# Kernel tuning notes

Measured on AMD Instinct MI355X. Metric: run time of the kernel, lower is better.

The kernel has to match this reference:

```python
import jax, jax.numpy as jnp
import numpy as np

N = 200000
E = 600000
C = 256


def setup_inputs() -> dict:
    key = jax.random.key(0)
    k1, k2, k3, k4, k5 = jax.random.split(key, 5)
    x = jax.random.normal(k1, (N, C), dtype=jnp.float32)
    sources = jax.random.randint(k2, (E,), 0, N, dtype=jnp.int64)
    targets = jax.random.randint(k3, (E,), 0, N, dtype=jnp.int64)
    norm = jax.random.uniform(k4, (N, 1), dtype=jnp.float32)
    # xavier_normal for [C, C]: std = sqrt(2 / (fan_in + fan_out))
    std = float(np.sqrt(2.0 / (C + C)))
    weight = jax.random.normal(k5, (C, C), dtype=jnp.float32) * std
    return {"x": x, "sources": sources, "targets": targets, "norm": norm, "weight": weight}


def reference(x, sources, targets, norm, weight):
    # out-of-place index_add: x + scatter_add(x[sources] -> targets)
    agg = x.at[targets].add(x[sources])  # [N, C]
    h = norm * agg                        # [N, C], norm broadcasts over channels
    return h @ weight                     # [N, C]
```

## Files before the change

### kernel.cpp

```cpp
#include <hip/hip_runtime.h>
#include <hip/hip_bf16.h>

#define NN 200000
#define NE 600000
#define CH 256
#define NBLK_SCAN 196

typedef short bf16x8 __attribute__((ext_vector_type(8)));
typedef float f32x4 __attribute__((ext_vector_type(4)));
typedef unsigned short ushort8v __attribute__((ext_vector_type(8)));

__device__ __forceinline__ unsigned short f2bf(float f) {
    unsigned int u = __builtin_bit_cast(unsigned int, f);
    u = (u + 0x7FFFu + ((u >> 16) & 1u)) >> 16;
    return (unsigned short)u;
}
__device__ __forceinline__ float bf2f(unsigned short u) {
    unsigned int v = ((unsigned int)u) << 16;
    return __builtin_bit_cast(float, v);
}

__global__ __launch_bounds__(256) void k_prep(const float* __restrict__ W,
                                              unsigned short* __restrict__ Wt,
                                              const int* __restrict__ te,
                                              int* __restrict__ deg) {
    const int t = blockIdx.x * 256 + threadIdx.x;
    const int S = gridDim.x * 256;
    for (int e = t; e < NE; e += S) atomicAdd(&deg[te[e]], 1);
    for (int i = t; i < CH * CH; i += S) {
        int j = i >> 8, k = i & 255;
        Wt[j * CH + k] = f2bf(W[k * CH + j]);
    }
}

__global__ __launch_bounds__(256) void k_scanA(const int* __restrict__ deg,
                                               int* __restrict__ off,
                                               int* __restrict__ bsum) {
    __shared__ int ts[256];
    int tid = threadIdx.x;
    int base = blockIdx.x * 1024 + tid * 4;
    int v[4];
#pragma unroll
    for (int j = 0; j < 4; ++j) {
        int idx = base + j;
        v[j] = (idx < NN) ? deg[idx] : 0;
    }
    int tsum = v[0] + v[1] + v[2] + v[3];
    ts[tid] = tsum;
    __syncthreads();
    int x = tsum;
    for (int ofs = 1; ofs < 256; ofs <<= 1) {
        int y = (tid >= ofs) ? ts[tid - ofs] : 0;
        __syncthreads();
        x += y;
        ts[tid] = x;
        __syncthreads();
    }
    int run = x - tsum;
#pragma unroll
    for (int j = 0; j < 4; ++j) {
        int idx = base + j;
        if (idx < NN) off[idx] = run;
        run += v[j];
    }
    if (tid == 255) bsum[blockIdx.x] = x;
}

__global__ __launch_bounds__(256) void k_scanB(int* __restrict__ bsum) {
    __shared__ int ts[256];
    int tid = threadIdx.x;
    int v = (tid < NBLK_SCAN) ? bsum[tid] : 0;
    ts[tid] = v;
    __syncthreads();
    int x = v;
    for (int ofs = 1; ofs < 256; ofs <<= 1) {
        int y = (tid >= ofs) ? ts[tid - ofs] : 0;
        __syncthreads();
        x += y;
        ts[tid] = x;
        __syncthreads();
    }
    if (tid < NBLK_SCAN) bsum[tid] = x - v;
}

__global__ __launch_bounds__(256) void k_scanC(int* __restrict__ off,
                                               const int* __restrict__ bsum,
                                               int* __restrict__ cur) {
    int tid = threadIdx.x;
    int base = blockIdx.x * 1024 + tid * 4;
    int bo = bsum[blockIdx.x];
#pragma unroll
    for (int j = 0; j < 4; ++j) {
        int idx = base + j;
        if (idx < NN) {
            int o = off[idx] + bo;
            off[idx] = o;
            cur[idx] = o;
        }
    }
}

__global__ void k_fill(const int* __restrict__ se, const int* __restrict__ te,
                       int* __restrict__ cur, int* __restrict__ elist) {
    int e = blockIdx.x * 256 + threadIdx.x;
    if (e < NE) {
        int t = te[e];
        int pos = atomicAdd(&cur[t], 1);
        elist[pos] = se[e];
    }
}

__global__ __launch_bounds__(256, 2) void k_zw(const float* __restrict__ x,
                                               const unsigned short* __restrict__ Wt,
                                               unsigned short* __restrict__ zbf) {
    __shared__ unsigned short lds_a[64 * CH];
    const int tid = threadIdx.x;
    const int wid = tid >> 6;
    const int lane = tid & 63;
    const int rb = blockIdx.x * 64;
    const int r16 = lane & 15;
    const int q = lane >> 4;

    const float* gx = x + (size_t)rb * CH;
#pragma unroll
    for (int i = 0; i < 8; ++i) {
        const int idx = i * 2048 + tid * 8;
        const int row = idx >> 8;
        const int col = idx & 255;
        float4 f0 = *reinterpret_cast<const float4*>(gx + idx);
        float4 f1 = *reinterpret_cast<const float4*>(gx + idx + 4);
        ushort8v w;
        w[0] = f2bf(f0.x); w[1] = f2bf(f0.y); w[2] = f2bf(f0.z); w[3] = f2bf(f0.w);
        w[4] = f2bf(f1.x); w[5] = f2bf(f1.y); w[6] = f2bf(f1.z); w[7] = f2bf(f1.w);
        const int gs = (col >> 3) ^ (row & 7);
        *reinterpret_cast<ushort8v*>(&lds_a[row * CH + gs * 8]) = w;
    }
    __syncthreads();

    f32x4 acc[4][4];
#pragma unroll
    for (int m = 0; m < 4; ++m)
#pragma unroll
        for (int nt = 0; nt < 4; ++nt) acc[m][nt] = (f32x4){0.f, 0.f, 0.f, 0.f};

    const unsigned short* wb = Wt + (size_t)(wid * 64 + r16) * CH + q * 8;

#pragma unroll
    for (int kk = 0; kk < 8; ++kk) {
        bf16x8 b[4];
#pragma unroll
        for (int nt = 0; nt < 4; ++nt)
            b[nt] = *reinterpret_cast<const bf16x8*>(wb + (size_t)nt * 16 * CH + kk * 32);
        bf16x8 a[4];
#pragma unroll
        for (int m = 0; m < 4; ++m) {
            const int lr = m * 16 + r16;
            const int idx = lr * CH + ((((kk * 4) + q) ^ (lr & 7)) << 3);
            a[m] = *reinterpret_cast<const bf16x8*>(&lds_a[idx]);
        }
#pragma unroll
        for (int m = 0; m < 4; ++m)
#pragma unroll
            for (int nt = 0; nt < 4; ++nt)
                acc[m][nt] = __builtin_amdgcn_mfma_f32_16x16x32_bf16(a[m], b[nt], acc[m][nt], 0, 0, 0);
    }

#pragma unroll
    for (int m = 0; m < 4; ++m) {
        const int crow = rb + m * 16 + q * 4;
#pragma unroll
        for (int nt = 0; nt < 4; ++nt) {
            unsigned short* po = zbf + (size_t)crow * CH + wid * 64 + nt * 16 + r16;
#pragma unroll
            for (int r = 0; r < 4; ++r) po[(size_t)r * CH] = f2bf(acc[m][nt][r]);
        }
    }
}

__global__ __launch_bounds__(256) void k_gout(const unsigned short* __restrict__ zbf,
                                              const int* __restrict__ off,
                                              const int* __restrict__ deg,
                                              const int* __restrict__ elist,
                                              const float* __restrict__ norm,
                                              float* __restrict__ out) {
    int wid = threadIdx.x >> 6;
    int lane = threadIdx.x & 63;
    int row = blockIdx.x * 4 + wid;
    if (row >= NN) return;
    int start = off[row];
    int d = deg[row];
    const int uo = lane * 4;
    ushort4 bv = *reinterpret_cast<const ushort4*>(zbf + (size_t)row * CH + uo);
    float ax = bf2f(bv.x), ay = bf2f(bv.y), az = bf2f(bv.z), aw = bf2f(bv.w);
    int e = 0;
    while (e < d) {
        int i0 = (e + 0 < d) ? elist[start + e + 0] : -1;
        int i1 = (e + 1 < d) ? elist[start + e + 1] : -1;
        int i2 = (e + 2 < d) ? elist[start + e + 2] : -1;
        int i3 = (e + 3 < d) ? elist[start + e + 3] : -1;
        int i4 = (e + 4 < d) ? elist[start + e + 4] : -1;
        int i5 = (e + 5 < d) ? elist[start + e + 5] : -1;
        int i6 = (e + 6 < d) ? elist[start + e + 6] : -1;
        int i7 = (e + 7 < d) ? elist[start + e + 7] : -1;
#define GACC(ii) if (ii >= 0) { \
            ushort4 v = *reinterpret_cast<const ushort4*>(zbf + (size_t)ii * CH + uo); \
            ax += bf2f(v.x); ay += bf2f(v.y); az += bf2f(v.z); aw += bf2f(v.w); }
        GACC(i0) GACC(i1) GACC(i2) GACC(i3) GACC(i4) GACC(i5) GACC(i6) GACC(i7)
#undef GACC
        e += 8;
    }
    const float nv = norm[row];
    float4 o;
    o.x = ax * nv; o.y = ay * nv; o.z = az * nv; o.w = aw * nv;
    *reinterpret_cast<float4*>(out + (size_t)row * CH + uo) = o;
}

__global__ __launch_bounds__(256, 4) void k_fgg(const float* __restrict__ x,
                                                const int* __restrict__ off,
                                                const int* __restrict__ deg,
                                                const int* __restrict__ elist,
                                                const float* __restrict__ norm,
                                                const unsigned short* __restrict__ Wt,
                                                float* __restrict__ out) {
    __shared__ unsigned short lds_a[64 * CH];
    const int tid = threadIdx.x;
    const int wid = tid >> 6;
    const int lane = tid & 63;
    const int rb = blockIdx.x * 64;
    const int rowbase = rb + wid * 16;
    const int r16 = lane & 15;
    const int q = lane >> 4;
    const int fo4 = lane * 4;

    const int offv = off[rowbase + r16];
    const int degv = deg[rowbase + r16];
    const float nv = norm[rb + lane];

    float4 acc[16];
#pragma unroll
    for (int r = 0; r < 16; ++r)
        acc[r] = *reinterpret_cast<const float4*>(x + (size_t)(rowbase + r) * CH + fo4);

#pragma unroll
    for (int r = 0; r < 16; ++r) {
        const int start = __shfl(offv, r);
        const int d = __shfl(degv, r);
        int e = 0;
        while (e < d) {
            int i0 = (e + 0 < d) ? elist[start + e + 0] : -1;
            int i1 = (e + 1 < d) ? elist[start + e + 1] : -1;
            int i2 = (e + 2 < d) ? elist[start + e + 2] : -1;
            int i3 = (e + 3 < d) ? elist[start + e + 3] : -1;
#define GACC(ii) if (ii >= 0) { \
            float4 v = *reinterpret_cast<const float4*>(x + (size_t)ii * CH + fo4); \
            acc[r].x += v.x; acc[r].y += v.y; acc[r].z += v.z; acc[r].w += v.w; }
            GACC(i0) GACC(i1) GACC(i2) GACC(i3)
#undef GACC
            e += 4;
        }
    }

    unsigned short* lb = lds_a + wid * 16 * CH;
#pragma unroll
    for (int r = 0; r < 16; ++r) {
        ushort4 w;
        w.x = f2bf(acc[r].x); w.y = f2bf(acc[r].y);
        w.z = f2bf(acc[r].z); w.w = f2bf(acc[r].w);
        const int gs = (lane >> 1) ^ (r & 7);
        *reinterpret_cast<ushort4*>(lb + r * CH + gs * 8 + (lane & 1) * 4) = w;
    }
    __syncthreads();

    f32x4 facc[4][4];
#pragma unroll
    for (int m = 0; m < 4; ++m)
#pragma unroll
        for (int nt = 0; nt < 4; ++nt) facc[m][nt] = (f32x4){0.f, 0.f, 0.f, 0.f};

    const unsigned short* wb = Wt + (size_t)(wid * 64 + r16) * CH + q * 8;

#pragma unroll
    for (int kk = 0; kk < 8; ++kk) {
        bf16x8 b[4];
#pragma unroll
        for (int nt = 0; nt < 4; ++nt)
            b[nt] = *reinterpret_cast<const bf16x8*>(wb + (size_t)nt * 16 * CH + kk * 32);
        bf16x8 a[4];
#pragma unroll
        for (int m = 0; m < 4; ++m) {
            const int lr = m * 16 + r16;
            const int idx = lr * CH + ((((kk * 4) + q) ^ (lr & 7)) << 3);
            a[m] = *reinterpret_cast<const bf16x8*>(&lds_a[idx]);
        }
#pragma unroll
        for (int m = 0; m < 4; ++m)
#pragma unroll
            for (int nt = 0; nt < 4; ++nt)
                facc[m][nt] = __builtin_amdgcn_mfma_f32_16x16x32_bf16(a[m], b[nt], facc[m][nt], 0, 0, 0);
    }

#pragma unroll
    for (int m = 0; m < 4; ++m) {
        const int crow = rb + m * 16 + q * 4;
#pragma unroll
        for (int nt = 0; nt < 4; ++nt) {
            float* po = out + (size_t)crow * CH + wid * 64 + nt * 16 + r16;
#pragma unroll
            for (int r = 0; r < 4; ++r) {
                const float nj = __shfl(nv, m * 16 + q * 4 + r);
                po[(size_t)r * CH] = facc[m][nt][r] * nj;
            }
        }
    }
}

extern "C" void kernel_launch(void* const* d_in, const int* in_sizes, int n_in,
                              void* d_out, int out_size, void* d_ws, size_t ws_size,
                              hipStream_t stream) {
    const float* x = (const float*)d_in[0];
    const int* se = (const int*)d_in[1];
    const int* te = (const int*)d_in[2];
    const float* norm = (const float*)d_in[3];
    const float* W = (const float*)d_in[4];
    float* out = (float*)d_out;

    char* ws = (char*)d_ws;
    unsigned short* Wt = (unsigned short*)ws;
    int* deg   = (int*)(ws + 131072);
    int* off   = (int*)(ws + 931072);
    int* cur   = (int*)(ws + 1731072);
    int* elist = (int*)(ws + 2531072);
    int* bsum  = (int*)(ws + 4931072);
    const size_t ZBF_OFF = 4932096;
    const size_t NEED = ZBF_OFF + (size_t)NN * CH * 2;
    const bool big = (ws_size >= NEED);
    unsigned short* zbf = (unsigned short*)(ws + ZBF_OFF);

    hipMemsetAsync(deg, 0, NN * sizeof(int), stream);
    k_prep<<<512, 256, 0, stream>>>(W, Wt, te, deg);
    k_scanA<<<NBLK_SCAN, 256, 0, stream>>>(deg, off, bsum);
    k_scanB<<<1, 256, 0, stream>>>(bsum);
    k_scanC<<<NBLK_SCAN, 256, 0, stream>>>(off, bsum, cur);
    k_fill<<<(NE + 255) / 256, 256, 0, stream>>>(se, te, cur, elist);
    if (big) {
        k_zw<<<NN / 64, 256, 0, stream>>>(x, Wt, zbf);
        k_gout<<<NN / 4, 256, 0, stream>>>(zbf, off, deg, elist, norm, out);
    } else {
        k_fgg<<<NN / 64, 256, 0, stream>>>(x, off, deg, elist, norm, Wt, out);
    }
}
```

Measured before the change: 279.1 us.

## Fold block-sum scan into scanC and double-buffer operand loads in k_zw

Removes the single-block k_scanB launch: each k_scanC block now redundantly scans all block sums in LDS and picks its own offset. k_zw issues all of its global x loads up front before converting them, and double-buffers the A (LDS) and B (global) MFMA operands across k-steps. Its occupancy hint is also raised from 2 to 3 waves. The aim is to cut one kernel launch and to hide load latency in the GEMM, at the cost of more registers that may not fit the higher occupancy target.

```diff
diff --git a/kernel.cpp b/kernel.cpp
--- a/kernel.cpp
+++ b/kernel.cpp
@@ -66,7 +66,9 @@
     if (tid == 255) bsum[blockIdx.x] = x;
 }
 
-__global__ __launch_bounds__(256) void k_scanB(int* __restrict__ bsum) {
+__global__ __launch_bounds__(256) void k_scanC(int* __restrict__ off,
+                                               const int* __restrict__ bsum,
+                                               int* __restrict__ cur) {
     __shared__ int ts[256];
     int tid = threadIdx.x;
     int v = (tid < NBLK_SCAN) ? bsum[tid] : 0;
@@ -80,15 +82,8 @@
         ts[tid] = x;
         __syncthreads();
     }
-    if (tid < NBLK_SCAN) bsum[tid] = x - v;
-}
-
-__global__ __launch_bounds__(256) void k_scanC(int* __restrict__ off,
-                                               const int* __restrict__ bsum,
-                                               int* __restrict__ cur) {
-    int tid = threadIdx.x;
+    const int bo = (blockIdx.x == 0) ? 0 : ts[blockIdx.x - 1];
     int base = blockIdx.x * 1024 + tid * 4;
-    int bo = bsum[blockIdx.x];
 #pragma unroll
     for (int j = 0; j < 4; ++j) {
         int idx = base + j;
@@ -110,7 +105,7 @@
     }
 }
 
-__global__ __launch_bounds__(256, 2) void k_zw(const float* __restrict__ x,
+__global__ __launch_bounds__(256, 3) void k_zw(const float* __restrict__ x,
                                                const unsigned short* __restrict__ Wt,
                                                unsigned short* __restrict__ zbf) {
     __shared__ unsigned short lds_a[64 * CH];
@@ -122,48 +117,62 @@
     const int q = lane >> 4;
 
     const float* gx = x + (size_t)rb * CH;
+    float4 st[16];
+#pragma unroll
+    for (int i = 0; i < 8; ++i) {
+        const int idx = i * 2048 + tid * 8;
+        st[2 * i]     = *reinterpret_cast<const float4*>(gx + idx);
+        st[2 * i + 1] = *reinterpret_cast<const float4*>(gx + idx + 4);
+    }
 #pragma unroll
     for (int i = 0; i < 8; ++i) {
         const int idx = i * 2048 + tid * 8;
         const int row = idx >> 8;
         const int col = idx & 255;
-        float4 f0 = *reinterpret_cast<const float4*>(gx + idx);
-        float4 f1 = *reinterpret_cast<const float4*>(gx + idx + 4);
         ushort8v w;
-        w[0] = f2bf(f0.x); w[1] = f2bf(f0.y); w[2] = f2bf(f0.z); w[3] = f2bf(f0.w);
-        w[4] = f2bf(f1.x); w[5] = f2bf(f1.y); w[6] = f2bf(f1.z); w[7] = f2bf(f1.w);
+        w[0] = f2bf(st[2 * i].x); w[1] = f2bf(st[2 * i].y);
+        w[2] = f2bf(st[2 * i].z); w[3] = f2bf(st[2 * i].w);
+        w[4] = f2bf(st[2 * i + 1].x); w[5] = f2bf(st[2 * i + 1].y);
+        w[6] = f2bf(st[2 * i + 1].z); w[7] = f2bf(st[2 * i + 1].w);
         const int gs = (col >> 3) ^ (row & 7);
         *reinterpret_cast<ushort8v*>(&lds_a[row * CH + gs * 8]) = w;
     }
     __syncthreads();
 
+    const unsigned short* wb = Wt + (size_t)(wid * 64 + r16) * CH + q * 8;
+#define LOADB(nt, kk) (*reinterpret_cast<const bf16x8*>(wb + (size_t)(nt) * 16 * CH + (kk) * 32))
+#define LOADA(m, kk) (*reinterpret_cast<const bf16x8*>(&lds_a[(m * 16 + r16) * CH + (((((kk) * 4) + q) ^ ((m * 16 + r16) & 7)) << 3)]))
+
+    bf16x8 ab[2][4], bb[2][4];
+#pragma unroll
+    for (int nt = 0; nt < 4; ++nt) bb[0][nt] = LOADB(nt, 0);
+#pragma unroll
+    for (int m = 0; m < 4; ++m) ab[0][m] = LOADA(m, 0);
+
     f32x4 acc[4][4];
 #pragma unroll
     for (int m = 0; m < 4; ++m)
 #pragma unroll
         for (int nt = 0; nt < 4; ++nt) acc[m][nt] = (f32x4){0.f, 0.f, 0.f, 0.f};
 
-    const unsigned short* wb = Wt + (size_t)(wid * 64 + r16) * CH + q * 8;
-
 #pragma unroll
     for (int kk = 0; kk < 8; ++kk) {
-        bf16x8 b[4];
-#pragma unroll
-        for (int nt = 0; nt < 4; ++nt)
-            b[nt] = *reinterpret_cast<const bf16x8*>(wb + (size_t)nt * 16 * CH + kk * 32);
-        bf16x8 a[4];
-#pragma unroll
-        for (int m = 0; m < 4; ++m) {
-            const int lr = m * 16 + r16;
-            const int idx = lr * CH + ((((kk * 4) + q) ^ (lr & 7)) << 3);
-            a[m] = *reinterpret_cast<const bf16x8*>(&lds_a[idx]);
+        const int cur = kk & 1;
+        const int nxt = cur ^ 1;
+        if (kk < 7) {
+#pragma unroll
+            for (int nt = 0; nt < 4; ++nt) bb[nxt][nt] = LOADB(nt, kk + 1);
+#pragma unroll
+            for (int m = 0; m < 4; ++m) ab[nxt][m] = LOADA(m, kk + 1);
         }
 #pragma unroll
         for (int m = 0; m < 4; ++m)
 #pragma unroll
             for (int nt = 0; nt < 4; ++nt)
-                acc[m][nt] = __builtin_amdgcn_mfma_f32_16x16x32_bf16(a[m], b[nt], acc[m][nt], 0, 0, 0);
-    }
+                acc[m][nt] = __builtin_amdgcn_mfma_f32_16x16x32_bf16(ab[cur][m], bb[cur][nt], acc[m][nt], 0, 0, 0);
+    }
+#undef LOADB
+#undef LOADA
 
 #pragma unroll
     for (int m = 0; m < 4; ++m) {
@@ -339,7 +348,6 @@
     hipMemsetAsync(deg, 0, NN * sizeof(int), stream);
     k_prep<<<512, 256, 0, stream>>>(W, Wt, te, deg);
     k_scanA<<<NBLK_SCAN, 256, 0, stream>>>(deg, off, bsum);
-    k_scanB<<<1, 256, 0, stream>>>(bsum);
     k_scanC<<<NBLK_SCAN, 256, 0, stream>>>(off, bsum, cur);
     k_fill<<<(NE + 255) / 256, 256, 0, stream>>>(se, te, cur, elist);
     if (big) {
```

After: 280.3 us. Within noise of the previous version (+0.4%).

## Fuse degree counting into GEMM, merge scan passes, widen GEMM tiles

Applied to the files above, without the earlier changes.

Folds the separate block-sum scan kernel into the final scan pass, with each block redoing the small 196-entry scan in LDS. Moves the edge-degree atomics into the z=xW GEMM kernel and splits the weight transpose into its own small kernel. Widens the GEMM block to 128 rows and 512 threads and stages the bf16 output through LDS for coalesced 16-byte stores. The goal is fewer launches and better store efficiency, at the cost of higher LDS use per block (64 KB), which may limit occupancy.

```diff
diff --git a/kernel.cpp b/kernel.cpp
--- a/kernel.cpp
+++ b/kernel.cpp
@@ -18,6 +18,11 @@
 __device__ __forceinline__ float bf2f(unsigned short u) {
     unsigned int v = ((unsigned int)u) << 16;
     return __builtin_bit_cast(float, v);
+}
+
+__global__ void k_wt(const float* __restrict__ W, unsigned short* __restrict__ Wt) {
+    int j = blockIdx.x, k = threadIdx.x;
+    Wt[j * CH + k] = f2bf(W[k * CH + j]);
 }
 
 __global__ __launch_bounds__(256) void k_prep(const float* __restrict__ W,
@@ -66,7 +71,9 @@
     if (tid == 255) bsum[blockIdx.x] = x;
 }
 
-__global__ __launch_bounds__(256) void k_scanB(int* __restrict__ bsum) {
+__global__ __launch_bounds__(256) void k_scanC(int* __restrict__ off,
+                                               const int* __restrict__ bsum,
+                                               int* __restrict__ cur) {
     __shared__ int ts[256];
     int tid = threadIdx.x;
     int v = (tid < NBLK_SCAN) ? bsum[tid] : 0;
@@ -80,15 +87,8 @@
         ts[tid] = x;
         __syncthreads();
     }
-    if (tid < NBLK_SCAN) bsum[tid] = x - v;
-}
-
-__global__ __launch_bounds__(256) void k_scanC(int* __restrict__ off,
-                                               const int* __restrict__ bsum,
-                                               int* __restrict__ cur) {
-    int tid = threadIdx.x;
+    const int bo = (blockIdx.x == 0) ? 0 : ts[blockIdx.x - 1];
     int base = blockIdx.x * 1024 + tid * 4;
-    int bo = bsum[blockIdx.x];
 #pragma unroll
     for (int j = 0; j < 4; ++j) {
         int idx = base + j;
@@ -110,25 +110,36 @@
     }
 }
 
-__global__ __launch_bounds__(256, 2) void k_zw(const float* __restrict__ x,
+__global__ __launch_bounds__(512, 4) void k_zw(const float* __restrict__ x,
                                                const unsigned short* __restrict__ Wt,
-                                               unsigned short* __restrict__ zbf) {
-    __shared__ unsigned short lds_a[64 * CH];
+                                               unsigned short* __restrict__ zbf,
+                                               const int* __restrict__ te,
+                                               int* __restrict__ deg) {
+    __shared__ unsigned short lds_a[128 * CH];
     const int tid = threadIdx.x;
     const int wid = tid >> 6;
     const int lane = tid & 63;
-    const int rb = blockIdx.x * 64;
+    const int wr = wid >> 2;
+    const int wc = wid & 3;
+    const int rb = blockIdx.x * 128;
     const int r16 = lane & 15;
     const int q = lane >> 4;
-
-    const float* gx = x + (size_t)rb * CH;
+    const int vr = min(128, NN - rb);
+
+    {
+        const long long e = (long long)blockIdx.x * 512 + tid;
+        if (e < NE) atomicAdd(&deg[te[e]], 1);
+    }
+
 #pragma unroll
     for (int i = 0; i < 8; ++i) {
-        const int idx = i * 2048 + tid * 8;
+        const int idx = i * 4096 + tid * 8;
         const int row = idx >> 8;
         const int col = idx & 255;
-        float4 f0 = *reinterpret_cast<const float4*>(gx + idx);
-        float4 f1 = *reinterpret_cast<const float4*>(gx + idx + 4);
+        const int srow = min(rb + row, NN - 1);
+        const float* src = x + (size_t)srow * CH + col;
+        float4 f0 = *reinterpret_cast<const float4*>(src);
+        float4 f1 = *reinterpret_cast<const float4*>(src + 4);
         ushort8v w;
         w[0] = f2bf(f0.x); w[1] = f2bf(f0.y); w[2] = f2bf(f0.z); w[3] = f2bf(f0.w);
         w[4] = f2bf(f1.x); w[5] = f2bf(f1.y); w[6] = f2bf(f1.z); w[7] = f2bf(f1.w);
@@ -143,7 +154,7 @@
 #pragma unroll
         for (int nt = 0; nt < 4; ++nt) acc[m][nt] = (f32x4){0.f, 0.f, 0.f, 0.f};
 
-    const unsigned short* wb = Wt + (size_t)(wid * 64 + r16) * CH + q * 8;
+    const unsigned short* wb = Wt + (size_t)(wc * 64 + r16) * CH + q * 8;
 
 #pragma unroll
     for (int kk = 0; kk < 8; ++kk) {
@@ -154,9 +165,9 @@
         bf16x8 a[4];
 #pragma unroll
         for (int m = 0; m < 4; ++m) {
-            const int lr = m * 16 + r16;
-            const int idx = lr * CH + ((((kk * 4) + q) ^ (lr & 7)) << 3);
-            a[m] = *reinterpret_cast<const bf16x8*>(&lds_a[idx]);
+            const int lr = wr * 64 + m * 16 + r16;
+            const int aidx = lr * CH + ((((kk * 4) + q) ^ (lr & 7)) << 3);
+            a[m] = *reinterpret_cast<const bf16x8*>(&lds_a[aidx]);
         }
 #pragma unroll
         for (int m = 0; m < 4; ++m)
@@ -165,15 +176,27 @@
                 acc[m][nt] = __builtin_amdgcn_mfma_f32_16x16x32_bf16(a[m], b[nt], acc[m][nt], 0, 0, 0);
     }
 
+    __syncthreads();
 #pragma unroll
     for (int m = 0; m < 4; ++m) {
-        const int crow = rb + m * 16 + q * 4;
 #pragma unroll
         for (int nt = 0; nt < 4; ++nt) {
-            unsigned short* po = zbf + (size_t)crow * CH + wid * 64 + nt * 16 + r16;
-#pragma unroll
-            for (int r = 0; r < 4; ++r) po[(size_t)r * CH] = f2bf(acc[m][nt][r]);
-        }
+            const int zr = wr * 64 + m * 16 + q * 4;
+            const int zc = wc * 64 + nt * 16 + r16;
+#pragma unroll
+            for (int r = 0; r < 4; ++r)
+                lds_a[(zr + r) * CH + zc] = f2bf(acc[m][nt][r]);
+        }
+    }
+    __syncthreads();
+    unsigned short* zdst = zbf + (size_t)rb * CH;
+#pragma unroll
+    for (int j = 0; j < 8; ++j) {
+        const int idx = j * 4096 + tid * 8;
+        const int row = idx >> 8;
+        if (row < vr)
+            *reinterpret_cast<ushort8v*>(zdst + idx) =
+                *reinterpret_cast<const ushort8v*>(&lds_a[idx]);
     }
 }
 
@@ -337,15 +360,18 @@
     unsigned short* zbf = (unsigned short*)(ws + ZBF_OFF);
 
     hipMemsetAsync(deg, 0, NN * sizeof(int), stream);
-    k_prep<<<512, 256, 0, stream>>>(W, Wt, te, deg);
-    k_scanA<<<NBLK_SCAN, 256, 0, stream>>>(deg, off, bsum);
-    k_scanB<<<1, 256, 0, stream>>>(bsum);
-    k_scanC<<<NBLK_SCAN, 256, 0, stream>>>(off, bsum, cur);
-    k_fill<<<(NE + 255) / 256, 256, 0, stream>>>(se, te, cur, elist);
     if (big) {
-        k_zw<<<NN / 64, 256, 0, stream>>>(x, Wt, zbf);
+        k_wt<<<CH, CH, 0, stream>>>(W, Wt);
+        k_zw<<<(NN + 127) / 128, 512, 0, stream>>>(x, Wt, zbf, te, deg);
+        k_scanA<<<NBLK_SCAN, 256, 0, stream>>>(deg, off, bsum);
+        k_scanC<<<NBLK_SCAN, 256, 0, stream>>>(off, bsum, cur);
+        k_fill<<<(NE + 255) / 256, 256, 0, stream>>>(se, te, cur, elist);
         k_gout<<<NN / 4, 256, 0, stream>>>(zbf, off, deg, elist, norm, out);
     } else {
+        k_prep<<<512, 256, 0, stream>>>(W, Wt, te, deg);
+        k_scanA<<<NBLK_SCAN, 256, 0, stream>>>(deg, off, bsum);
+        k_scanC<<<NBLK_SCAN, 256, 0, stream>>>(off, bsum, cur);
+        k_fill<<<(NE + 255) / 256, 256, 0, stream>>>(se, te, cur, elist);
         k_fgg<<<NN / 64, 256, 0, stream>>>(x, off, deg, elist, norm, Wt, out);
     }
 }
```

Result: faster. 263.2 us (-5.7%).

## Persistent double-buffered x@W GEMM with fused degree count and merged scan

Applied to the files above, without the earlier changes.

Turns k_zw into a persistent kernel of 512 blocks that loops over 32-row tiles. Each next tile of x is staged into LDS with async global_load_lds double buffering, the W fragments stay in registers for the whole kernel, and fp32 is converted to bf16 at LDS read time. Degree counting moves into the GEMM kernel so the atomics overlap with the GEMM. The separate scanB launch is removed by having each scanC block redo the small block-sum scan, and the W transpose becomes its own tiny kernel. This cuts launches and the exposed load latency, at the cost of heavy register use (32 bf16x8 B fragments) and twice the LDS footprint from keeping fp32 tiles.

```diff
diff --git a/kernel.cpp b/kernel.cpp
--- a/kernel.cpp
+++ b/kernel.cpp
@@ -5,6 +5,8 @@
 #define NE 600000
 #define CH 256
 #define NBLK_SCAN 196
+#define ZW_GRID 512
+#define ZW_TILES 6250
 
 typedef short bf16x8 __attribute__((ext_vector_type(8)));
 typedef float f32x4 __attribute__((ext_vector_type(4)));
@@ -18,6 +20,11 @@
 __device__ __forceinline__ float bf2f(unsigned short u) {
     unsigned int v = ((unsigned int)u) << 16;
     return __builtin_bit_cast(float, v);
+}
+
+__global__ void k_wt(const float* __restrict__ W, unsigned short* __restrict__ Wt) {
+    int j = blockIdx.x, k = threadIdx.x;
+    Wt[j * CH + k] = f2bf(W[k * CH + j]);
 }
 
 __global__ __launch_bounds__(256) void k_prep(const float* __restrict__ W,
@@ -66,7 +73,9 @@
     if (tid == 255) bsum[blockIdx.x] = x;
 }
 
-__global__ __launch_bounds__(256) void k_scanB(int* __restrict__ bsum) {
+__global__ __launch_bounds__(256) void k_scanC(int* __restrict__ off,
+                                               const int* __restrict__ bsum,
+                                               int* __restrict__ cur) {
     __shared__ int ts[256];
     int tid = threadIdx.x;
     int v = (tid < NBLK_SCAN) ? bsum[tid] : 0;
@@ -80,15 +89,8 @@
         ts[tid] = x;
         __syncthreads();
     }
-    if (tid < NBLK_SCAN) bsum[tid] = x - v;
-}
-
-__global__ __launch_bounds__(256) void k_scanC(int* __restrict__ off,
-                                               const int* __restrict__ bsum,
-                                               int* __restrict__ cur) {
-    int tid = threadIdx.x;
+    const int bo = (blockIdx.x == 0) ? 0 : ts[blockIdx.x - 1];
     int base = blockIdx.x * 1024 + tid * 4;
-    int bo = bsum[blockIdx.x];
 #pragma unroll
     for (int j = 0; j < 4; ++j) {
         int idx = base + j;
@@ -112,69 +114,97 @@
 
 __global__ __launch_bounds__(256, 2) void k_zw(const float* __restrict__ x,
                                                const unsigned short* __restrict__ Wt,
-                                               unsigned short* __restrict__ zbf) {
-    __shared__ unsigned short lds_a[64 * CH];
+                                               unsigned short* __restrict__ zbf,
+                                               const int* __restrict__ te,
+                                               int* __restrict__ deg) {
+    __shared__ float lds[2][32 * CH];
     const int tid = threadIdx.x;
     const int wid = tid >> 6;
     const int lane = tid & 63;
-    const int rb = blockIdx.x * 64;
     const int r16 = lane & 15;
     const int q = lane >> 4;
 
-    const float* gx = x + (size_t)rb * CH;
-#pragma unroll
-    for (int i = 0; i < 8; ++i) {
-        const int idx = i * 2048 + tid * 8;
-        const int row = idx >> 8;
-        const int col = idx & 255;
-        float4 f0 = *reinterpret_cast<const float4*>(gx + idx);
-        float4 f1 = *reinterpret_cast<const float4*>(gx + idx + 4);
-        ushort8v w;
-        w[0] = f2bf(f0.x); w[1] = f2bf(f0.y); w[2] = f2bf(f0.z); w[3] = f2bf(f0.w);
-        w[4] = f2bf(f1.x); w[5] = f2bf(f1.y); w[6] = f2bf(f1.z); w[7] = f2bf(f1.w);
-        const int gs = (col >> 3) ^ (row & 7);
-        *reinterpret_cast<ushort8v*>(&lds_a[row * CH + gs * 8]) = w;
-    }
-    __syncthreads();
-
-    f32x4 acc[4][4];
-#pragma unroll
-    for (int m = 0; m < 4; ++m)
-#pragma unroll
-        for (int nt = 0; nt < 4; ++nt) acc[m][nt] = (f32x4){0.f, 0.f, 0.f, 0.f};
-
-    const unsigned short* wb = Wt + (size_t)(wid * 64 + r16) * CH + q * 8;
-
-#pragma unroll
-    for (int kk = 0; kk < 8; ++kk) {
-        bf16x8 b[4];
-#pragma unroll
-        for (int nt = 0; nt < 4; ++nt)
-            b[nt] = *reinterpret_cast<const bf16x8*>(wb + (size_t)nt * 16 * CH + kk * 32);
-        bf16x8 a[4];
-#pragma unroll
-        for (int m = 0; m < 4; ++m) {
-            const int lr = m * 16 + r16;
-            const int idx = lr * CH + ((((kk * 4) + q) ^ (lr & 7)) << 3);
-            a[m] = *reinterpret_cast<const bf16x8*>(&lds_a[idx]);
-        }
-#pragma unroll
-        for (int m = 0; m < 4; ++m)
+#define STAGE(buf, tile)                                                                  \
+    {                                                                                     \
+        const float* src = x + (size_t)(tile) * 32 * CH;                                  \
+        _Pragma("unroll")                                                                 \
+        for (int i = 0; i < 8; ++i) {                                                     \
+            const int fi = i * 1024 + tid * 4;                                            \
+            const int row = fi >> 8;                                                      \
+            const int g = (fi & 255) >> 2;                                                \
+            const int sg = g ^ (row & 7);                                                 \
+            __builtin_amdgcn_global_load_lds(                                             \
+                (const __attribute__((address_space(1))) void*)(src + row * CH + sg * 4), \
+                (__attribute__((address_space(3))) void*)(&lds[buf][fi]), 16, 0, 0);      \
+        }                                                                                 \
+    }
+
+    int t = blockIdx.x;
+    STAGE(0, t)
+
+    bf16x8 breg[8][4];
+    {
+        const unsigned short* wb = Wt + (size_t)(wid * 64 + r16) * CH + q * 8;
+#pragma unroll
+        for (int kk = 0; kk < 8; ++kk)
 #pragma unroll
             for (int nt = 0; nt < 4; ++nt)
-                acc[m][nt] = __builtin_amdgcn_mfma_f32_16x16x32_bf16(a[m], b[nt], acc[m][nt], 0, 0, 0);
-    }
-
-#pragma unroll
-    for (int m = 0; m < 4; ++m) {
-        const int crow = rb + m * 16 + q * 4;
-#pragma unroll
-        for (int nt = 0; nt < 4; ++nt) {
-            unsigned short* po = zbf + (size_t)crow * CH + wid * 64 + nt * 16 + r16;
-#pragma unroll
-            for (int r = 0; r < 4; ++r) po[(size_t)r * CH] = f2bf(acc[m][nt][r]);
-        }
-    }
+                breg[kk][nt] = *reinterpret_cast<const bf16x8*>(wb + (size_t)nt * 16 * CH + kk * 32);
+    }
+
+    for (int e = blockIdx.x * 256 + tid; e < NE; e += ZW_GRID * 256)
+        atomicAdd(&deg[te[e]], 1);
+
+    int cur = 0;
+    for (; t < ZW_TILES; t += ZW_GRID) {
+        const int tn = t + ZW_GRID;
+        if (tn < ZW_TILES) STAGE(cur ^ 1, tn)
+        __syncthreads();
+
+        f32x4 acc[2][4];
+#pragma unroll
+        for (int m = 0; m < 2; ++m)
+#pragma unroll
+            for (int nt = 0; nt < 4; ++nt) acc[m][nt] = (f32x4){0.f, 0.f, 0.f, 0.f};
+
+#pragma unroll
+        for (int kk = 0; kk < 8; ++kk) {
+            bf16x8 a[2];
+#pragma unroll
+            for (int m = 0; m < 2; ++m) {
+                const int lr = m * 16 + r16;
+                const int sw = lr & 7;
+                const float* lp = &lds[cur][lr * CH];
+                const int g0 = kk * 8 + q * 2;
+                f32x4 lo = *reinterpret_cast<const f32x4*>(lp + ((g0 ^ sw) << 2));
+                f32x4 hi = *reinterpret_cast<const f32x4*>(lp + (((g0 + 1) ^ sw) << 2));
+                a[m][0] = (short)f2bf(lo[0]); a[m][1] = (short)f2bf(lo[1]);
+                a[m][2] = (short)f2bf(lo[2]); a[m][3] = (short)f2bf(lo[3]);
+                a[m][4] = (short)f2bf(hi[0]); a[m][5] = (short)f2bf(hi[1]);
+                a[m][6] = (short)f2bf(hi[2]); a[m][7] = (short)f2bf(hi[3]);
+            }
+#pragma unroll
+            for (int m = 0; m < 2; ++m)
+#pragma unroll
+                for (int nt = 0; nt < 4; ++nt)
+                    acc[m][nt] = __builtin_amdgcn_mfma_f32_16x16x32_bf16(a[m], breg[kk][nt], acc[m][nt], 0, 0, 0);
+        }
+
+        const int rb = t * 32;
+#pragma unroll
+        for (int m = 0; m < 2; ++m) {
+#pragma unroll
+            for (int nt = 0; nt < 4; ++nt) {
+                unsigned short* po = zbf + (size_t)(rb + m * 16 + q * 4) * CH
+                                   + wid * 64 + nt * 16 + r16;
+#pragma unroll
+                for (int r = 0; r < 4; ++r) po[(size_t)r * CH] = f2bf(acc[m][nt][r]);
+            }
+        }
+        __syncthreads();
+        cur ^= 1;
+    }
+#undef STAGE
 }
 
 __global__ __launch_bounds__(256) void k_gout(const unsigned short* __restrict__ zbf,
@@ -337,15 +367,18 @@
     unsigned short* zbf = (unsigned short*)(ws + ZBF_OFF);
 
     hipMemsetAsync(deg, 0, NN * sizeof(int), stream);
-    k_prep<<<512, 256, 0, stream>>>(W, Wt, te, deg);
-    k_scanA<<<NBLK_SCAN, 256, 0, stream>>>(deg, off, bsum);
-    k_scanB<<<1, 256, 0, stream>>>(bsum);
-    k_scanC<<<NBLK_SCAN, 256, 0, stream>>>(off, bsum, cur);
-    k_fill<<<(NE + 255) / 256, 256, 0, stream>>>(se, te, cur, elist);
     if (big) {
-        k_zw<<<NN / 64, 256, 0, stream>>>(x, Wt, zbf);
+        k_wt<<<CH, CH, 0, stream>>>(W, Wt);
+        k_zw<<<ZW_GRID, 256, 0, stream>>>(x, Wt, zbf, te, deg);
+        k_scanA<<<NBLK_SCAN, 256, 0, stream>>>(deg, off, bsum);
+        k_scanC<<<NBLK_SCAN, 256, 0, stream>>>(off, bsum, cur);
+        k_fill<<<(NE + 255) / 256, 256, 0, stream>>>(se, te, cur, elist);
         k_gout<<<NN / 4, 256, 0, stream>>>(zbf, off, deg, elist, norm, out);
     } else {
+        k_prep<<<512, 256, 0, stream>>>(W, Wt, te, deg);
+        k_scanA<<<NBLK_SCAN, 256, 0, stream>>>(deg, off, bsum);
+        k_scanC<<<NBLK_SCAN, 256, 0, stream>>>(off, bsum, cur);
+        k_fill<<<(NE + 255) / 256, 256, 0, stream>>>(se, te, cur, elist);
         k_fgg<<<NN / 64, 256, 0, stream>>>(x, off, deg, elist, norm, Wt, out);
     }
 }
```

New measurement: 238.3 us. 14.6% less time.
